# Kernel tuning notes

Measured on AMD Instinct MI355X. Metric: run time of the kernel, lower is better.

## Reference

```python
import jax, jax.numpy as jnp
import numpy as np

HEADS, DIM_HEAD = 8, 64  # per init_kwargs


def cdist(x, w):
    """Euclidean distance between rows of x [..., n, d] and w [m, d] -> [..., n, m].
    Matches torch.cdist (non-squared) / L2DistanceLinear(squared=False)."""
    sq = (x * x).sum(-1, keepdims=True) + (w * w).sum(-1) - 2.0 * (x @ w.T)
    return jnp.sqrt(jnp.maximum(sq, 0.0))


def setup_inputs() -> dict:
    key = jax.random.key(0)
    k1, k2, k3 = jax.random.split(key, 3)
    B, N, D = 4, 2048, 512
    dim_inner = HEADS * DIM_HEAD  # 512
    x = jax.random.normal(k1, (B, N, D), dtype=jnp.float32)
    w_qkv = jax.random.normal(k2, (3 * dim_inner, D), dtype=jnp.float32)
    w_out = jax.random.normal(k3, (D, dim_inner), dtype=jnp.float32)
    return {"x": x, "w_qkv": w_qkv, "w_out": w_out}


def reference(x, w_qkv, w_out):
    B, N, D = x.shape
    scale = DIM_HEAD ** -0.5

    # L2-distance QKV projection (cdist, non-squared, no negate/bias)
    qkv = cdist(x, w_qkv)                                  # [B, N, 3*H*DH]
    qkv = qkv.reshape(B, N, 3, HEADS, DIM_HEAD).transpose(2, 0, 3, 1, 4)  # [3, B, H, N, DH]
    q, k, v = qkv[0], qkv[1], qkv[2]

    # neg squared-L2 attention scores: -(||q||^2 + ||k||^2 - 2 q.k)
    q_sq = (q * q).sum(-1)                                 # [B, H, N]
    k_sq = (k * k).sum(-1)                                 # [B, H, N]
    dots = jnp.einsum('bhid,bhjd->bhij', q, k)             # [B, H, N, N]
    sim = -(q_sq[..., :, None] + k_sq[..., None, :] - 2.0 * dots) * scale

    attn = jax.nn.softmax(sim, axis=-1)
    out = jnp.einsum('bhij,bhjd->bhid', attn, v)           # [B, H, N, DH]
    out = out.transpose(0, 2, 1, 3).reshape(B, N, HEADS * DIM_HEAD)

    # L2-distance output projection
    return cdist(out, w_out)                               # [B, N, D]
```

## Files before the change

### kernel.cpp

```cpp
#include <hip/hip_runtime.h>
#include <stdint.h>

typedef float v4f  __attribute__((ext_vector_type(4)));
typedef float v16f __attribute__((ext_vector_type(16)));
typedef short v8s  __attribute__((ext_vector_type(8)));
typedef uint32_t u32;

#define DEVI static __device__ __forceinline__

DEVI unsigned short f2bf(float f) {
    u32 u = __builtin_bit_cast(u32, f);
    u = (u + 0x7fffu + ((u >> 16) & 1u)) >> 16;
    return (unsigned short)u;
}
DEVI float bf2f(unsigned short h) {
    u32 u = ((u32)h) << 16;
    return __builtin_bit_cast(float, u);
}

DEVI float fexp2(float x) {
#if __has_builtin(__builtin_amdgcn_exp2f)
    return __builtin_amdgcn_exp2f(x);
#else
    float r;
    asm("v_exp_f32 %0, %1" : "=v"(r) : "v"(x));
    return r;
#endif
}

template <typename T>
DEVI void async16(const T* g, T* l) {
    __builtin_amdgcn_global_load_lds(
        (const __attribute__((address_space(1))) u32*)g,
        (__attribute__((address_space(3))) u32*)l, 16, 0, 0);
}

DEVI v4f bmfma(v8s a, v8s b, v4f c) {
    return __builtin_amdgcn_mfma_f32_16x16x32_bf16(a, b, c, 0, 0, 0);
}
DEVI v16f bmfma32(v8s a, v8s b, v16f c) {
    return __builtin_amdgcn_mfma_f32_32x32x16_bf16(a, b, c, 0, 0, 0);
}

#if __has_builtin(__builtin_amdgcn_permlane32_swap)
#define HAVE_PLSWAP 1
typedef unsigned int v2u __attribute__((ext_vector_type(2)));
#endif

DEVI void swap32(u32 a, u32 b, u32& lo, u32& hi) {
#ifdef HAVE_PLSWAP
    v2u r = __builtin_amdgcn_permlane32_swap(a, b, false, false);
    lo = r.x; hi = r.y;
#else
    u32 ax = __shfl_xor(a, 32), bx = __shfl_xor(b, 32);
    int hh = (threadIdx.x & 63) >> 5;
    lo = hh ? bx : a;
    hi = hh ? b : ax;
#endif
}

static const size_t HSZ = 32ull * 2048 * 64;

__launch_bounds__(256, 2)
__global__ void prep_all(const float* __restrict__ X, const float* __restrict__ WQ,
                         const float* __restrict__ WO,
                         unsigned short* __restrict__ Xb, unsigned short* __restrict__ WQb,
                         unsigned short* __restrict__ WOb,
                         float* __restrict__ xsq, float* __restrict__ wqsq,
                         float* __restrict__ wosq, float* __restrict__ wors)
{
    const int bid = blockIdx.x;
    const int w = threadIdx.x >> 6, lane = threadIdx.x & 63;
    const float* src; unsigned short* dst; float* Sq; float* Rs = nullptr;
    int r;
    if (bid < 2048)      { src = X;  dst = Xb;  Sq = xsq;  r = bid * 4 + w; }
    else if (bid < 2432) { src = WQ; dst = WQb; Sq = wqsq; r = (bid - 2048) * 4 + w; }
    else                 { src = WO; dst = WOb; Sq = wosq; Rs = wors; r = (bid - 2432) * 4 + w; }

    const float* xr = src + (size_t)r * 512 + lane * 8;
    float4 a = *(const float4*)xr;
    float4 c = *(const float4*)(xr + 4);
    float s = a.x*a.x + a.y*a.y + a.z*a.z + a.w*a.w
            + c.x*c.x + c.y*c.y + c.z*c.z + c.w*c.w;
    float sm = a.x + a.y + a.z + a.w + c.x + c.y + c.z + c.w;
    uint4 pkv;
    unsigned short* e = (unsigned short*)&pkv;
    e[0] = f2bf(a.x); e[1] = f2bf(a.y); e[2] = f2bf(a.z); e[3] = f2bf(a.w);
    e[4] = f2bf(c.x); e[5] = f2bf(c.y); e[6] = f2bf(c.z); e[7] = f2bf(c.w);
    *(uint4*)(dst + (size_t)r * 512 + lane * 8) = pkv;
#pragma unroll
    for (int d = 32; d > 0; d >>= 1) {
        s  += __shfl_xor(s, d);
        sm += __shfl_xor(sm, d);
    }
    if (lane == 0) { Sq[r] = s; if (Rs) Rs[r] = sm; }
}

__launch_bounds__(256, 2)
__global__ void gemm_cdist(const unsigned short* __restrict__ A,
                           const unsigned short* __restrict__ B,
                           const float* __restrict__ Asq,
                           const float* __restrict__ Bsq,
                           unsigned short* __restrict__ QKV,
                           float* __restrict__ Ksqc)
{
    __shared__ unsigned short lsm[4 * 8192];
    const int t = threadIdx.x;
    const int lane = t & 63, w = t >> 6;
    const int low = lane & 15, quad = lane >> 4;
    const int wm = w & 1, wn = w >> 1;
    const int tM = blockIdx.x * 128, tN = blockIdx.y * 128;

    v4f acc[4][4];
#pragma unroll
    for (int a = 0; a < 4; ++a)
#pragma unroll
        for (int b = 0; b < 4; ++b) acc[a][b] = (v4f){0.f, 0.f, 0.f, 0.f};

    int kstage = 0;
    auto STAGE = [&](int buf) {
        unsigned short* lA = lsm + buf * 8192;
        unsigned short* lB = lA + 4096;
#pragma unroll
        for (int is = 0; is < 2; ++is) {
            int slot = is * 256 + t;
            int r = slot >> 2, bp = slot & 3, bs = bp ^ (r & 3);
            async16(A + (size_t)(tM + r) * 512 + kstage + bs * 8, lA + slot * 8);
            async16(B + (size_t)(tN + r) * 512 + kstage + bs * 8, lB + slot * 8);
        }
        kstage += 32;
    };

    STAGE(0);
    STAGE(1);

#pragma unroll
    for (int iter = 0; iter < 16; ++iter) {
        if (iter <= 13) STAGE((iter + 2) & 3);
        if (iter <= 13)      asm volatile("s_waitcnt vmcnt(8)" ::: "memory");
        else if (iter == 14) asm volatile("s_waitcnt vmcnt(4)" ::: "memory");
        else                 asm volatile("s_waitcnt vmcnt(0)" ::: "memory");
        __builtin_amdgcn_s_barrier();
        __builtin_amdgcn_sched_barrier(0);

        const unsigned short* lA = lsm + (iter & 3) * 8192;
        const unsigned short* lB = lA + 4096;

        v8s bfr[4];
#pragma unroll
        for (int ns = 0; ns < 4; ++ns) {
            int row = wn * 64 + ns * 16 + low;
            bfr[ns] = *(const v8s*)(lB + (row * 4 + (quad ^ (row & 3))) * 8);
        }
#pragma unroll
        for (int ms = 0; ms < 4; ++ms) {
            int row = wm * 64 + ms * 16 + low;
            v8s af = *(const v8s*)(lA + (row * 4 + (quad ^ (row & 3))) * 8);
#pragma unroll
            for (int ns = 0; ns < 4; ++ns)
                acc[ms][ns] = bmfma(af, bfr[ns], acc[ms][ns]);
        }
    }

    const int tt = tN >> 9;
    if (tt != 2) {
#pragma unroll
        for (int ms = 0; ms < 4; ++ms) {
#pragma unroll
            for (int reg = 0; reg < 4; ++reg) {
                const int row = tM + wm * 64 + ms * 16 + quad * 4 + reg;
                const int b = row >> 11, i = row & 2047;
                float kacc = 0.f;
#pragma unroll
                for (int ns = 0; ns < 4; ++ns) {
                    const int col = tN + wn * 64 + ns * 16 + low;
                    float dot = acc[ms][ns][reg];
                    float val = sqrtf(fmaxf(Asq[row] + Bsq[col] - 2.f * dot, 0.f)) - 32.f;
                    int h = (col >> 6) & 7, d = col & 63, bh = b * 8 + h;
                    if (tt == 0) {
                        QKV[((size_t)bh * 2048 + i) * 64 + d] =
                            f2bf(val * 0.36067376022224085f);
                    } else {
                        QKV[HSZ + ((size_t)bh * 2048 + i) * 64 + d] = f2bf(val);
                        kacc += val * val;
                    }
                }
                if (tt == 1) {
#pragma unroll
                    for (int d = 1; d < 16; d <<= 1) kacc += __shfl_xor(kacc, d);
                    if (low == 0) {
                        int h = ((tN + wn * 64) >> 6) & 7;
                        Ksqc[(size_t)(b * 8 + h) * 2048 + i] = -kacc * 0.18033688011112042f;
                    }
                }
            }
        }
    } else {
        u32 packed[4][4][2];
#pragma unroll
        for (int ms = 0; ms < 4; ++ms)
#pragma unroll
            for (int ns = 0; ns < 4; ++ns) {
                const int col = tN + wn * 64 + ns * 16 + low;
                float bs_ = Bsq[col];
#pragma unroll
                for (int rp = 0; rp < 2; ++rp) {
                    u32 pk = 0;
#pragma unroll
                    for (int sub = 0; sub < 2; ++sub) {
                        int reg = rp * 2 + sub;
                        int row = tM + wm * 64 + ms * 16 + quad * 4 + reg;
                        float val = sqrtf(fmaxf(Asq[row] + bs_
                                                - 2.f * acc[ms][ns][reg], 0.f)) - 32.f;
                        pk |= (u32)f2bf(val) << (16 * sub);
                    }
                    packed[ms][ns][rp] = pk;
                }
            }
        u32* lT32 = (u32*)lsm;
#pragma unroll
        for (int p = 0; p < 2; ++p) {
            __syncthreads();
            if (wm == p) {
#pragma unroll
                for (int ms = 0; ms < 4; ++ms)
#pragma unroll
                    for (int ns = 0; ns < 4; ++ns) {
                        int cl = wn * 64 + ns * 16 + low;
#pragma unroll
                        for (int rp = 0; rp < 2; ++rp)
                            lT32[cl * 36 + ms * 8 + quad * 2 + rp] = packed[ms][ns][rp];
                    }
            }
            __syncthreads();
#pragma unroll
            for (int cc = 0; cc < 4; ++cc) {
                int col = cc * 32 + (t >> 3);
                int i0 = (t & 7) * 8;
                uint4 vvv = *(const uint4*)(lsm + col * 72 + i0);
                int colg = tN + col;
                int h = (colg >> 6) & 7, d = colg & 63;
                int rowg = tM + p * 64 + i0;
                int b = rowg >> 11, i = rowg & 2047;
                *(uint4*)(QKV + 2 * HSZ
                          + ((size_t)((b * 8 + h) * 64 + d)) * 2048 + i) = vvv;
            }
        }
    }
    (void)0;
}

__launch_bounds__(256, 2)
__global__ void flash_attn(const unsigned short* __restrict__ Q,
                           const unsigned short* __restrict__ K,
                           const unsigned short* __restrict__ VT,
                           const float* __restrict__ Ksqc,
                           unsigned short* __restrict__ OP,
                           float* __restrict__ Osqp)
{
    __shared__ unsigned short lK[2][64 * 64];
    __shared__ unsigned short lV[2][64 * 64];
    __shared__ float lKqA[2048];
    const int t = threadIdx.x, lane = t & 63, w = t >> 6;
    const int i31 = lane & 31, h = lane >> 5;
    const int bid = blockIdx.x;
    const int bh = (bid & 7) * 4 + (bid >> 7);
    const int qt = (bid >> 3) & 15;
    const size_t base = (size_t)bh * (2048 * 64);
    const int row0 = qt * 128 + w * 32;

    v8s qfr[4];
#pragma unroll
    for (int kt = 0; kt < 4; ++kt)
        qfr[kt] = *(const v8s*)(Q + base + (size_t)(row0 + i31) * 64 + kt * 16 + h * 8);

    v16f o[2];
    float lacc = 0.f;
#pragma unroll
    for (int dt = 0; dt < 2; ++dt)
#pragma unroll
        for (int r = 0; r < 16; ++r) o[dt][r] = 0.f;

    const unsigned short* kg = K + base;
    const unsigned short* vg = VT + (size_t)bh * 64 * 2048;
    const float* kqg = Ksqc + (size_t)bh * 2048;

    auto STAGE = [&](int buf) {
#pragma unroll
        for (int is = 0; is < 2; ++is) {
            int slot = is * 256 + t;
            int r = slot >> 3, bp = slot & 7, bs = bp ^ (r & 7);
            async16(kg + (size_t)r * 64 + bs * 8, &lK[buf][slot * 8]);
        }
#pragma unroll
        for (int is = 0; is < 2; ++is) {
            int slot = is * 256 + t;
            int r = slot >> 3, bp = slot & 7, bs = bp ^ (r & 7);
            async16(vg + (size_t)r * 2048 + bs * 8, &lV[buf][slot * 8]);
        }
        kg += 64 * 64; vg += 64;
    };

#pragma unroll
    for (int is = 0; is < 2; ++is) {
        int slot = is * 256 + t;
        async16(kqg + slot * 4, lKqA + slot * 4);
    }
    STAGE(0);
    __syncthreads();

#pragma unroll 2
    for (int iter = 0; iter < 32; ++iter) {
        const int c = iter & 1;

        asm volatile("s_waitcnt lgkmcnt(0)" ::: "memory");
        __builtin_amdgcn_s_barrier();
        if (iter < 31) {
            STAGE(1 - c);
            asm volatile("s_waitcnt vmcnt(4)" ::: "memory");
        } else {
            asm volatile("s_waitcnt vmcnt(0)" ::: "memory");
        }
        __builtin_amdgcn_s_barrier();
        __builtin_amdgcn_sched_barrier(0);

        const int jrow0 = i31, jrow1 = 32 + i31;
        v8s kf0[4], kf1[4];
#pragma unroll
        for (int kt = 0; kt < 4; ++kt) {
            kf0[kt] = *(const v8s*)(&lK[c][(jrow0 * 8 + ((2 * kt + h) ^ (jrow0 & 7))) * 8]);
            kf1[kt] = *(const v8s*)(&lK[c][(jrow1 * 8 + ((2 * kt + h) ^ (jrow1 & 7))) * 8]);
        }
        v16f sa0, sa1;
#pragma unroll
        for (int r1 = 0; r1 < 4; ++r1) {
            v4f kq0 = *(const v4f*)(&lKqA[iter * 64 + r1 * 8 + h * 4]);
            v4f kq1 = *(const v4f*)(&lKqA[iter * 64 + 32 + r1 * 8 + h * 4]);
#pragma unroll
            for (int u = 0; u < 4; ++u) {
                sa0[4 * r1 + u] = kq0[u];
                sa1[4 * r1 + u] = kq1[u];
            }
        }
#pragma unroll
        for (int kt = 0; kt < 4; ++kt) sa0 = bmfma32(kf0[kt], qfr[kt], sa0);
#pragma unroll
        for (int kt = 0; kt < 4; ++kt) sa1 = bmfma32(kf1[kt], qfr[kt], sa1);

        u32 pk0[8];
#pragma unroll
        for (int r1 = 0; r1 < 4; ++r1) {
            float p0 = fexp2(sa0[4 * r1 + 0]);
            float p1 = fexp2(sa0[4 * r1 + 1]);
            float p2 = fexp2(sa0[4 * r1 + 2]);
            float p3 = fexp2(sa0[4 * r1 + 3]);
            lacc += (p0 + p1) + (p2 + p3);
            pk0[2 * r1] = __builtin_amdgcn_perm(
                __builtin_bit_cast(u32, p1), __builtin_bit_cast(u32, p0),
                0x07060302u);
            pk0[2 * r1 + 1] = __builtin_amdgcn_perm(
                __builtin_bit_cast(u32, p3), __builtin_bit_cast(u32, p2),
                0x07060302u);
        }
#pragma unroll
        for (int c2 = 0; c2 < 2; ++c2) {
            const int jb = 2 * c2;
            v8s vf[2];
#pragma unroll
            for (int dt = 0; dt < 2; ++dt) {
                const int drow = dt * 32 + i31;
                vf[dt] = *(const v8s*)(&lV[c][(drow * 8 + ((jb + h) ^ (drow & 7))) * 8]);
            }
            uint4 dd;
            swap32(pk0[4 * c2 + 0], pk0[4 * c2 + 2], dd.x, dd.z);
            swap32(pk0[4 * c2 + 1], pk0[4 * c2 + 3], dd.y, dd.w);
            v8s af = __builtin_bit_cast(v8s, dd);
            o[0] = bmfma32(af, vf[0], o[0]);
            o[1] = bmfma32(af, vf[1], o[1]);
        }

        u32 pk1[8];
#pragma unroll
        for (int r1 = 0; r1 < 4; ++r1) {
            float p0 = fexp2(sa1[4 * r1 + 0]);
            float p1 = fexp2(sa1[4 * r1 + 1]);
            float p2 = fexp2(sa1[4 * r1 + 2]);
            float p3 = fexp2(sa1[4 * r1 + 3]);
            lacc += (p0 + p1) + (p2 + p3);
            pk1[2 * r1] = __builtin_amdgcn_perm(
                __builtin_bit_cast(u32, p1), __builtin_bit_cast(u32, p0),
                0x07060302u);
            pk1[2 * r1 + 1] = __builtin_amdgcn_perm(
                __builtin_bit_cast(u32, p3), __builtin_bit_cast(u32, p2),
                0x07060302u);
        }
#pragma unroll
        for (int c2 = 0; c2 < 2; ++c2) {
            const int jb = 4 + 2 * c2;
            v8s vf[2];
#pragma unroll
            for (int dt = 0; dt < 2; ++dt) {
                const int drow = dt * 32 + i31;
                vf[dt] = *(const v8s*)(&lV[c][(drow * 8 + ((jb + h) ^ (drow & 7))) * 8]);
            }
            uint4 dd;
            swap32(pk1[4 * c2 + 0], pk1[4 * c2 + 2], dd.x, dd.z);
            swap32(pk1[4 * c2 + 1], pk1[4 * c2 + 3], dd.y, dd.w);
            v8s af = __builtin_bit_cast(v8s, dd);
            o[0] = bmfma32(af, vf[0], o[0]);
            o[1] = bmfma32(af, vf[1], o[1]);
        }
    }

    const int b = bh >> 3, hh = bh & 7;
    lacc += __shfl_xor(lacc, 32);
    unsigned short* ob = OP + ((size_t)(b * 2048 + row0)) * 512 + hh * 64;
    float* osq = Osqp + (size_t)hh * 8192 + b * 2048 + row0;
#pragma unroll
    for (int r = 0; r < 16; ++r) {
        const int rl = (r & 3) + 8 * (r >> 2) + 4 * h;
        float inv = 1.f / __shfl(lacc, rl);
        unsigned short e0 = f2bf(o[0][r] * inv);
        unsigned short e1 = f2bf(o[1][r] * inv);
        ob[(size_t)rl * 512 + i31] = e0;
        ob[(size_t)rl * 512 + 32 + i31] = e1;
        float f0 = bf2f(e0) + 32.f, f1 = bf2f(e1) + 32.f;
        float s = f0 * f0 + f1 * f1;
        s += __shfl_xor(s, 1);  s += __shfl_xor(s, 2);  s += __shfl_xor(s, 4);
        s += __shfl_xor(s, 8);  s += __shfl_xor(s, 16);
        if (i31 == 0) osq[rl] = s;
    }
}

__launch_bounds__(256, 2)
__global__ void gemm_out(const unsigned short* __restrict__ A,
                         const unsigned short* __restrict__ B,
                         const float* __restrict__ Osqp,
                         const float* __restrict__ Bsq,
                         const float* __restrict__ Brs,
                         float* __restrict__ OUT)
{
    __shared__ unsigned short lA[2][128 * 64];
    __shared__ unsigned short lB[2][64 * 64];
    __shared__ float lAsq[128];
    const int t = threadIdx.x;
    const int lane = t & 63, w = t >> 6;
    const int low = lane & 15, quad = lane >> 4;
    const int wm = w & 1, wn = w >> 1;
    const int tM = blockIdx.x * 128, tN = blockIdx.y * 64;

    if (t < 128) {
        float s = 0.f;
#pragma unroll
        for (int hh = 0; hh < 8; ++hh) s += Osqp[(size_t)hh * 8192 + tM + t];
        lAsq[t] = s;
    }

    v4f acc[4][2];
#pragma unroll
    for (int a = 0; a < 4; ++a)
#pragma unroll
        for (int b = 0; b < 2; ++b) acc[a][b] = (v4f){0.f, 0.f, 0.f, 0.f};

    int kstage = 0;
    auto STAGE = [&](int buf) {
#pragma unroll
        for (int is = 0; is < 4; ++is) {
            int slot = is * 256 + t;
            int r = slot >> 3, bp = slot & 7, bs = bp ^ (r & 7);
            async16(A + (size_t)(tM + r) * 512 + kstage + bs * 8, &lA[buf][slot * 8]);
        }
#pragma unroll
        for (int is = 0; is < 2; ++is) {
            int slot = is * 256 + t;
            int r = slot >> 3, bp = slot & 7, bs = bp ^ (r & 7);
            async16(B + (size_t)(tN + r) * 512 + kstage + bs * 8, &lB[buf][slot * 8]);
        }
        kstage += 64;
    };

    STAGE(0);
    __syncthreads();

#pragma unroll 2
    for (int iter = 0; iter < 8; ++iter) {
        const int c = iter & 1;
        if (iter < 7) STAGE(1 - c);

        v8s bfr[2][2];
#pragma unroll
        for (int ns = 0; ns < 2; ++ns) {
            int row = wn * 32 + ns * 16 + low;
#pragma unroll
            for (int kc = 0; kc < 2; ++kc)
                bfr[ns][kc] = *(const v8s*)(&lB[c][(row * 8 + ((kc * 4 + quad) ^ (row & 7))) * 8]);
        }
#pragma unroll
        for (int ms = 0; ms < 4; ++ms) {
            int row = wm * 64 + ms * 16 + low;
            v8s af0 = *(const v8s*)(&lA[c][(row * 8 + ((0 + quad) ^ (row & 7))) * 8]);
            v8s af1 = *(const v8s*)(&lA[c][(row * 8 + ((4 + quad) ^ (row & 7))) * 8]);
#pragma unroll
            for (int ns = 0; ns < 2; ++ns) {
                acc[ms][ns] = bmfma(af0, bfr[ns][0], acc[ms][ns]);
                acc[ms][ns] = bmfma(af1, bfr[ns][1], acc[ms][ns]);
            }
        }
        __syncthreads();
    }

#pragma unroll
    for (int ms = 0; ms < 4; ++ms) {
#pragma unroll
        for (int ns = 0; ns < 2; ++ns) {
#pragma unroll
            for (int reg = 0; reg < 4; ++reg) {
                int rloc = wm * 64 + ms * 16 + quad * 4 + reg;
                int row = tM + rloc;
                int col = tN + wn * 32 + ns * 16 + low;
                float val = sqrtf(fmaxf(lAsq[rloc] + Bsq[col]
                                        - 2.f * (acc[ms][ns][reg] + 32.f * Brs[col]), 0.f));
                OUT[(size_t)row * 512 + col] = val;
            }
        }
    }
}

extern "C" void kernel_launch(void* const* d_in, const int* in_sizes, int n_in,
                              void* d_out, int out_size, void* d_ws, size_t ws_size,
                              hipStream_t stream)
{
    const float* x    = (const float*)d_in[0];
    const float* wqkv = (const float*)d_in[1];
    const float* wout = (const float*)d_in[2];
    float* out = (float*)d_out;

    char* ws = (char*)d_ws;
    size_t off = 0;
    auto alloc = [&](size_t bytes) -> void* {
        void* p = ws + off;
        off += (bytes + 255) & ~(size_t)255;
        return p;
    };
    unsigned short* xb   = (unsigned short*)alloc(8192ull * 512 * 2);
    unsigned short* wqb  = (unsigned short*)alloc(1536ull * 512 * 2);
    unsigned short* wob  = (unsigned short*)alloc(512ull * 512 * 2);
    unsigned short* qkv  = (unsigned short*)alloc(3ull * HSZ * 2);
    unsigned short* outp = (unsigned short*)alloc(8192ull * 512 * 2);
    float* xsq  = (float*)alloc(8192 * 4);
    float* wqsq = (float*)alloc(1536 * 4);
    float* wosq = (float*)alloc(512 * 4);
    float* wors = (float*)alloc(512 * 4);
    float* ksqc = (float*)alloc(65536ull * 4);
    float* osqp = (float*)alloc(8ull * 8192 * 4);

    prep_all<<<2560, 256, 0, stream>>>(x, wqkv, wout, xb, wqb, wob,
                                       xsq, wqsq, wosq, wors);

    gemm_cdist<<<dim3(64, 12), 256, 0, stream>>>(xb, wqb, xsq, wqsq, qkv, ksqc);
    flash_attn<<<512, 256, 0, stream>>>(qkv, qkv + HSZ, qkv + 2 * HSZ,
                                        ksqc, outp, osqp);
    gemm_out<<<dim3(64, 8), 256, 0, stream>>>(outp, wob, osqp, wosq, wors, out);
}
```

Before: 160.0 us.

## Deepen flash attention K/V pipeline to four LDS buffers with prefetch distance two

Replaces the double-buffered K/V staging in the flash attention kernel with a four-slot ring buffer that prefetches two tiles ahead. The loop is restructured into an unrolled group of four with one barrier per iteration instead of two, and an explicit epilogue drains the last tiles. This hides more global-load latency and removes a barrier, but doubles K/V LDS use (about 64KB plus the Ksq array), which may hurt the two-blocks-per-CU occupancy target.

```diff
diff --git a/kernel.cpp b/kernel.cpp
--- a/kernel.cpp
+++ b/kernel.cpp
@@ -258,8 +258,8 @@
                            unsigned short* __restrict__ OP,
                            float* __restrict__ Osqp)
 {
-    __shared__ unsigned short lK[2][64 * 64];
-    __shared__ unsigned short lV[2][64 * 64];
+    __shared__ unsigned short lK[4][64 * 64];
+    __shared__ unsigned short lV[4][64 * 64];
     __shared__ float lKqA[2048];
     const int t = threadIdx.x, lane = t & 63, w = t >> 6;
     const int i31 = lane & 31, h = lane >> 5;
@@ -301,41 +301,19 @@
         kg += 64 * 64; vg += 64;
     };
 
-#pragma unroll
-    for (int is = 0; is < 2; ++is) {
-        int slot = is * 256 + t;
-        async16(kqg + slot * 4, lKqA + slot * 4);
-    }
-    STAGE(0);
-    __syncthreads();
-
-#pragma unroll 2
-    for (int iter = 0; iter < 32; ++iter) {
-        const int c = iter & 1;
-
-        asm volatile("s_waitcnt lgkmcnt(0)" ::: "memory");
-        __builtin_amdgcn_s_barrier();
-        if (iter < 31) {
-            STAGE(1 - c);
-            asm volatile("s_waitcnt vmcnt(4)" ::: "memory");
-        } else {
-            asm volatile("s_waitcnt vmcnt(0)" ::: "memory");
-        }
-        __builtin_amdgcn_s_barrier();
-        __builtin_amdgcn_sched_barrier(0);
-
+    auto COMPUTE = [&](int cb, int kqoff) {
         const int jrow0 = i31, jrow1 = 32 + i31;
         v8s kf0[4], kf1[4];
 #pragma unroll
         for (int kt = 0; kt < 4; ++kt) {
-            kf0[kt] = *(const v8s*)(&lK[c][(jrow0 * 8 + ((2 * kt + h) ^ (jrow0 & 7))) * 8]);
-            kf1[kt] = *(const v8s*)(&lK[c][(jrow1 * 8 + ((2 * kt + h) ^ (jrow1 & 7))) * 8]);
+            kf0[kt] = *(const v8s*)(&lK[cb][(jrow0 * 8 + ((2 * kt + h) ^ (jrow0 & 7))) * 8]);
+            kf1[kt] = *(const v8s*)(&lK[cb][(jrow1 * 8 + ((2 * kt + h) ^ (jrow1 & 7))) * 8]);
         }
         v16f sa0, sa1;
 #pragma unroll
         for (int r1 = 0; r1 < 4; ++r1) {
-            v4f kq0 = *(const v4f*)(&lKqA[iter * 64 + r1 * 8 + h * 4]);
-            v4f kq1 = *(const v4f*)(&lKqA[iter * 64 + 32 + r1 * 8 + h * 4]);
+            v4f kq0 = *(const v4f*)(&lKqA[kqoff + r1 * 8 + h * 4]);
+            v4f kq1 = *(const v4f*)(&lKqA[kqoff + 32 + r1 * 8 + h * 4]);
 #pragma unroll
             for (int u = 0; u < 4; ++u) {
                 sa0[4 * r1 + u] = kq0[u];
@@ -369,7 +347,7 @@
 #pragma unroll
             for (int dt = 0; dt < 2; ++dt) {
                 const int drow = dt * 32 + i31;
-                vf[dt] = *(const v8s*)(&lV[c][(drow * 8 + ((jb + h) ^ (drow & 7))) * 8]);
+                vf[dt] = *(const v8s*)(&lV[cb][(drow * 8 + ((jb + h) ^ (drow & 7))) * 8]);
             }
             uint4 dd;
             swap32(pk0[4 * c2 + 0], pk0[4 * c2 + 2], dd.x, dd.z);
@@ -401,7 +379,7 @@
 #pragma unroll
             for (int dt = 0; dt < 2; ++dt) {
                 const int drow = dt * 32 + i31;
-                vf[dt] = *(const v8s*)(&lV[c][(drow * 8 + ((jb + h) ^ (drow & 7))) * 8]);
+                vf[dt] = *(const v8s*)(&lV[cb][(drow * 8 + ((jb + h) ^ (drow & 7))) * 8]);
             }
             uint4 dd;
             swap32(pk1[4 * c2 + 0], pk1[4 * c2 + 2], dd.x, dd.z);
@@ -410,7 +388,45 @@
             o[0] = bmfma32(af, vf[0], o[0]);
             o[1] = bmfma32(af, vf[1], o[1]);
         }
-    }
+    };
+
+#pragma unroll
+    for (int is = 0; is < 2; ++is) {
+        int slot = is * 256 + t;
+        async16(kqg + slot * 4, lKqA + slot * 4);
+    }
+    STAGE(0);
+    STAGE(1);
+
+#pragma unroll 1
+    for (int g = 0; g < 7; ++g) {
+#pragma unroll
+        for (int u = 0; u < 4; ++u) {
+            STAGE((u + 2) & 3);
+            asm volatile("s_waitcnt vmcnt(8)" ::: "memory");
+            __builtin_amdgcn_s_barrier();
+            __builtin_amdgcn_sched_barrier(0);
+            COMPUTE(u, (g * 4 + u) * 64);
+        }
+    }
+    STAGE(2);
+    asm volatile("s_waitcnt vmcnt(8)" ::: "memory");
+    __builtin_amdgcn_s_barrier();
+    __builtin_amdgcn_sched_barrier(0);
+    COMPUTE(0, 28 * 64);
+    STAGE(3);
+    asm volatile("s_waitcnt vmcnt(8)" ::: "memory");
+    __builtin_amdgcn_s_barrier();
+    __builtin_amdgcn_sched_barrier(0);
+    COMPUTE(1, 29 * 64);
+    asm volatile("s_waitcnt vmcnt(4)" ::: "memory");
+    __builtin_amdgcn_s_barrier();
+    __builtin_amdgcn_sched_barrier(0);
+    COMPUTE(2, 30 * 64);
+    asm volatile("s_waitcnt vmcnt(0)" ::: "memory");
+    __builtin_amdgcn_s_barrier();
+    __builtin_amdgcn_sched_barrier(0);
+    COMPUTE(3, 31 * 64);
 
     const int b = bh >> 3, hh = bh & 7;
     lacc += __shfl_xor(lacc, 32);
```

After: 160.2 us. Within noise of the previous version (+0.1%).
